# Kernel optimization log

Hardware: AMD Instinct MI355X
Metric: run time of the kernel (lower is better)

Reference implementation:

```python
import jax, jax.numpy as jnp
import numpy as np

# Dimensions
B, NIN, P, K, D, F = 8, 4096, 1024, 16, 2, 64
CPF, C, DM = 64, 128, 2
CIN = CPF + F
BN_EPS = 1e-3  # Keras BatchNormalization default epsilon


def _bn(x, prm):
    # inference-mode batchnorm; prm is (4, C): gamma, beta, moving_mean, moving_var
    g, b, m, v = prm
    return g * (x - m) * jax.lax.rsqrt(v + BN_EPS) + b


def setup_inputs() -> dict:
    key = jax.random.key(0)
    ks = jax.random.split(key, 24)
    s = 0.05
    def rn(k, shape):
        return jax.random.normal(k, shape, jnp.float32) * s
    def bn_prm(k, c):
        kg, kb, km, kv = jax.random.split(k, 4)
        return jnp.stack([
            1.0 + 0.1 * jax.random.normal(kg, (c,), jnp.float32),
            0.1 * jax.random.normal(kb, (c,), jnp.float32),
            0.1 * jax.random.normal(km, (c,), jnp.float32),
            jax.random.uniform(kv, (c,), jnp.float32, 0.5, 1.5),
        ])
    inputs = jax.random.normal(ks[0], (B, NIN, 3 + F), jnp.float32)
    return {
        "inputs": inputs,
        "W_pf1": rn(ks[1], (3, CPF)), "b_pf1": rn(ks[2], (CPF,)), "bn_pf1": bn_prm(ks[3], CPF),
        "W_pf2": rn(ks[4], (CPF, CPF)), "b_pf2": rn(ks[5], (CPF,)), "bn_pf2": bn_prm(ks[6], CPF),
        "W_c1": rn(ks[7], (K, 3, K * K)), "b_c1": rn(ks[8], (K * K,)), "bn_c1": bn_prm(ks[9], K * K),
        "W_c2": rn(ks[10], (K, K, K)), "b_c2": rn(ks[11], (K * K,)), "bn_c2": bn_prm(ks[12], K * K),
        "W_c3": rn(ks[13], (K, K, K)), "b_c3": rn(ks[14], (K * K,)), "bn_c3": bn_prm(ks[15], K * K),
        "W_df": rn(ks[16], (K, CIN, DM)), "W_pw": rn(ks[17], (CIN * DM, C)),
        "b_f": rn(ks[18], (C,)), "bn_f": bn_prm(ks[19], C),
    }


def reference(inputs, W_pf1, b_pf1, bn_pf1, W_pf2, b_pf2, bn_pf2,
              W_c1, b_c1, bn_c1, W_c2, b_c2, bn_c2, W_c3, b_c3, bn_c3,
              W_df, W_pw, b_f, bn_f):
    p = inputs[:, :, :3]              # (B, NIN, 3) positions
    q = p[:, :P, :]                   # (B, P, 3) 'random' sampled query points
    # knn_indices_general(q, p, K*D, sorted=True): squared-distance top-k
    d2 = (q * q).sum(-1)[:, :, None] + (p * p).sum(-1)[:, None, :] \
         - 2.0 * jnp.einsum('bqc,bpc->bqp', q, p)          # (B, P, NIN)
    _, idx_kd = jax.lax.top_k(-d2, K * D)                  # ascending distance
    idx = idx_kd[:, :, ::D]                                # dilation -> (B, P, K)
    gathered = jnp.take_along_axis(
        inputs, idx.reshape(B, P * K)[:, :, None], axis=1).reshape(B, P, K, 3 + F)
    p_nb = gathered[..., :3] - q[:, :, None, :]            # (B, P, K, 3) local coords
    f_nb = gathered[..., 3:]                               # (B, P, K, F)
    # pos -> feature: Dense, BN, Dense, BN (no activation in source)
    h = _bn(p_nb @ W_pf1 + b_pf1, bn_pf1)
    h = _bn(h @ W_pf2 + b_pf2, bn_pf2)
    feat = jnp.concatenate([h, f_nb], axis=-1)             # (B, P, K, CIN)
    # Conv2D(K*K, (1,K), elu) + BN: contraction over neighbor axis
    x = _bn(jax.nn.elu(jnp.einsum('bnjc,jco->bno', p_nb, W_c1) + b_c1), bn_c1)
    x = x.reshape(B, P, K, K)
    # DepthwiseConv2D((1,K), mult=K, elu) + BN; Keras channel order c*mult+m
    x = _bn(jax.nn.elu(jnp.einsum('bnwc,wcm->bncm', x, W_c2).reshape(B, P, K * K) + b_c2), bn_c2)
    x = x.reshape(B, P, K, K)
    x = _bn(jax.nn.elu(jnp.einsum('bnwc,wcm->bncm', x, W_c3).reshape(B, P, K * K) + b_c3), bn_c3)
    x = x.reshape(B, P, K, K)
    # per-point KxK X-transform on gathered features
    feat = jnp.einsum('bnij,bnjc->bnic', x, feat)          # (B, P, K, CIN)
    # SeparableConv2D(C, (1,K), mult=DM, elu) + BN; width axis collapses
    dw = jnp.einsum('bnjc,jcm->bncm', feat, W_df).reshape(B, P, CIN * DM)
    out = _bn(jax.nn.elu(dw @ W_pw + b_f), bn_f)           # (B, P, C)
    return jnp.concatenate([q, out], axis=-1)              # (B, P, 3 + C)
```

## Files before the change

kernel.cpp:

```cpp
#include <hip/hip_runtime.h>
#include <math.h>

#define B_    8
#define NIN_  4096
#define P_    1024
#define K_    16
#define F_    64
#define CH_   67
#define CPF_  64
#define CIN_  128
#define C_    128

#define S_PF1  0
#define SH_PF1 64
#define S_PF2  128
#define SH_PF2 192
#define S_C1   256
#define SH_C1  512
#define S_C2   768
#define SH_C2  1024
#define S_C3   1280
#define SH_C3  1536
#define S_F    1792
#define SH_F   1920
#define M_OFF  2048
#define C0_OFF 2240

#define WS_PTS_OFF  16384
#define WS_IDX_OFF  (WS_PTS_OFF + B_ * NIN_ * 16)
#define WS_DWL_OFF  (WS_IDX_OFF + B_ * P_ * K_ * 4)

__device__ __forceinline__ float rlf(float x, int l) {
    return __int_as_float(__builtin_amdgcn_readlane(__float_as_int(x), l));
}
__device__ __forceinline__ float eluf(float z) {
    return z > 0.f ? z : expm1f(z);
}
__device__ __forceinline__ float dpp_shr1_f(float x) {
    return __int_as_float(__builtin_amdgcn_update_dpp(
        __float_as_int(x), __float_as_int(x), 0x138, 0xF, 0xF, false));
}
__device__ __forceinline__ int dpp_shr1_i(int x) {
    return __builtin_amdgcn_update_dpp(x, x, 0x138, 0xF, 0xF, false);
}

__global__ void bn_prep(const float* __restrict__ bn_pf1, const float* __restrict__ bn_pf2,
                        const float* __restrict__ bn_c1,  const float* __restrict__ bn_c2,
                        const float* __restrict__ bn_c3,  const float* __restrict__ bn_f,
                        const float* __restrict__ Wpf1,   const float* __restrict__ bpf1,
                        const float* __restrict__ Wpf2,   const float* __restrict__ bpf2,
                        float* __restrict__ wsf) {
    int t = threadIdx.x;
    {
        const float* src; int nch, c, so, sho;
        if (t < 64)       { src = bn_pf1; nch = 64;  c = t;        so = S_PF1; sho = SH_PF1; }
        else if (t < 128) { src = bn_pf2; nch = 64;  c = t - 64;   so = S_PF2; sho = SH_PF2; }
        else if (t < 384) { src = bn_c1;  nch = 256; c = t - 128;  so = S_C1;  sho = SH_C1; }
        else if (t < 640) { src = bn_c2;  nch = 256; c = t - 384;  so = S_C2;  sho = SH_C2; }
        else if (t < 896) { src = bn_c3;  nch = 256; c = t - 640;  so = S_C3;  sho = SH_C3; }
        else              { src = bn_f;   nch = 128; c = t - 896;  so = S_F;   sho = SH_F;  }
        float g = src[c], b = src[nch + c], m = src[2 * nch + c], v = src[3 * nch + c];
        float s = g * rsqrtf(v + 1e-3f);
        wsf[so + c]  = s;
        wsf[sho + c] = b - m * s;
    }
    __syncthreads();
    if (t < 64) {
        int o = t;
        float s2 = wsf[S_PF2 + o], t2 = wsf[SH_PF2 + o];
        float m0 = 0.f, m1 = 0.f, m2 = 0.f, cc = 0.f;
        for (int c = 0; c < 64; ++c) {
            float s1 = wsf[S_PF1 + c], t1 = wsf[SH_PF1 + c];
            float d1 = s1 * bpf1[c] + t1;
            float w2 = Wpf2[c * 64 + o];
            m0 += Wpf1[0 * 64 + c] * s1 * w2;
            m1 += Wpf1[1 * 64 + c] * s1 * w2;
            m2 += Wpf1[2 * 64 + c] * s1 * w2;
            cc += d1 * w2;
        }
        wsf[M_OFF + 0 * 64 + o] = m0 * s2;
        wsf[M_OFF + 1 * 64 + o] = m1 * s2;
        wsf[M_OFF + 2 * 64 + o] = m2 * s2;
        wsf[C0_OFF + o]         = cc * s2 + bpf2[o] * s2 + t2;
    }
}

__global__ __launch_bounds__(256) void pack_pts(const float* __restrict__ inp,
                                                float4* __restrict__ pts) {
    int i = blockIdx.x * 256 + threadIdx.x;
    if (i < B_ * NIN_) {
        const float* r = inp + (size_t)i * CH_;
        float x = r[0], y = r[1], z = r[2];
        float pp = __fadd_rn(__fadd_rn(__fmul_rn(x, x), __fmul_rn(y, y)),
                             __fmul_rn(z, z));
        pts[i] = make_float4(x, y, z, pp);
    }
}

__global__ __launch_bounds__(256) void knn_kernel(const float4* __restrict__ pts,
                                                  int* __restrict__ idxo) {
    const int wid  = (blockIdx.x << 2) | (threadIdx.x >> 6);
    const int lane = threadIdx.x & 63;
    const float4* bp = pts + ((size_t)(wid >> 10) << 12);
    const int qi = wid & 1023;

    const float4 q = bp[qi];
    const float qq = q.w;

    float4 p = bp[lane];
    float d;
    {
        float e = __fadd_rn(__fadd_rn(__fmul_rn(q.x, p.x), __fmul_rn(q.y, p.y)),
                            __fmul_rn(q.z, p.z));
        d = __fsub_rn(__fadd_rn(qq, p.w), __fmul_rn(2.0f, e));
    }
    int ii = lane;
#pragma unroll
    for (int k = 2; k <= 64; k <<= 1) {
#pragma unroll
        for (int j = k >> 1; j > 0; j >>= 1) {
            float od = __shfl_xor(d, j);
            int   oi = __shfl_xor(ii, j);
            bool keepmin = (((lane & k) == 0) == ((lane & j) == 0));
            bool ol = (od < d) || (od == d && oi < ii);
            bool take = keepmin ? ol : !ol;
            if (take) { d = od; ii = oi; }
        }
    }
    float bd = d;
    int   bi = ii;
    float kth = rlf(bd, 31);

    float4 pn = bp[64 + lane];
    for (int j0 = 64; j0 < NIN_; j0 += 64) {
        p = pn;
        if (j0 + 64 < NIN_) pn = bp[j0 + 64 + lane];
        float e  = __fadd_rn(__fadd_rn(__fmul_rn(q.x, p.x), __fmul_rn(q.y, p.y)),
                             __fmul_rn(q.z, p.z));
        float d2 = __fsub_rn(__fadd_rn(qq, p.w), __fmul_rn(2.0f, e));

        unsigned long long m = __ballot(d2 < kth);
        if (m) {
            do {
                int c = __builtin_ctzll(m);
                m &= m - 1;
                float dc = rlf(d2, c);
                int   ic = j0 + c;
                float prev  = dpp_shr1_f(bd);
                int   previ = dpp_shr1_i(bi);
                bool  shift = (bd > dc);
                bool  ins   = shift && ((lane == 0) || (prev <= dc));
                if (shift) { bd = prev; bi = previ; }
                if (ins)   { bd = dc;   bi = ic;    }
            } while (m);
            kth = rlf(bd, 31);
        }
    }

    if (lane < 32 && !(lane & 1)) {
        idxo[((size_t)wid << 4) | (lane >> 1)] = bi;
    }
}

__global__ __launch_bounds__(256) void p1_kernel(
    const float* __restrict__ inp, const int* __restrict__ idx,
    const float* __restrict__ Wc1,  const float* __restrict__ bc1,
    const float* __restrict__ Wc2,  const float* __restrict__ bc2,
    const float* __restrict__ Wc3,  const float* __restrict__ bc3,
    const float* __restrict__ Wdf,  const float* __restrict__ wsf,
    float* __restrict__ dwl, float* __restrict__ out) {

    __shared__ float xS[4][2][256];
    __shared__ float yS[4][2][256];

    const int w   = threadIdx.x >> 6;
    const int l   = threadIdx.x & 63;
    const int ngA = blockIdx.x * 8 + w * 2;
    const int ngB = ngA + 1;
    const int b   = ngA >> 10;
    const float* brow = inp + (size_t)b * NIN_ * CH_;
    const int* ipA = idx + (size_t)ngA * K_;
    const int* ipB = idx + (size_t)ngB * K_;

    const int nA = ngA & 1023, nB = ngB & 1023;
    const float q0A = brow[(size_t)nA * CH_ + 0];
    const float q1A = brow[(size_t)nA * CH_ + 1];
    const float q2A = brow[(size_t)nA * CH_ + 2];
    const float q0B = brow[(size_t)nB * CH_ + 0];
    const float q1B = brow[(size_t)nB * CH_ + 1];
    const float q2B = brow[(size_t)nB * CH_ + 2];

    float pdA, pdB;
    {
        int k3 = (l * 21846) >> 16;
        k3 = (k3 > 15) ? 15 : k3;
        int d3 = l - ((k3 << 1) + k3);
        d3 = (d3 > 2) ? 2 : d3;
        int nblA = ipA[k3];
        int nblB = ipB[k3];
        float vA = 0.f, vB = 0.f;
        if (l < 48) {
            vA = brow[(size_t)nblA * CH_ + d3];
            vB = brow[(size_t)nblB * CH_ + d3];
        }
        float qvA = (d3 == 0) ? q0A : ((d3 == 1) ? q1A : q2A);
        float qvB = (d3 == 0) ? q0B : ((d3 == 1) ? q1B : q2B);
        pdA = vA - qvA;
        pdB = vB - qvB;
    }

    {
        float4 accA = *reinterpret_cast<const float4*>(bc1 + 4 * l);
        float4 accB = accA;
#pragma unroll 4
        for (int t4 = 0; t4 < 12; ++t4) {
            const float* wb = Wc1 + (size_t)(t4 * 4) * 256 + 4 * l;
            float4 w0 = *reinterpret_cast<const float4*>(wb);
            float4 w1 = *reinterpret_cast<const float4*>(wb + 256);
            float4 w2 = *reinterpret_cast<const float4*>(wb + 512);
            float4 w3 = *reinterpret_cast<const float4*>(wb + 768);
            float a0 = rlf(pdA, 4 * t4 + 0), a1 = rlf(pdA, 4 * t4 + 1);
            float a2 = rlf(pdA, 4 * t4 + 2), a3 = rlf(pdA, 4 * t4 + 3);
            accA.x += a0 * w0.x + a1 * w1.x + a2 * w2.x + a3 * w3.x;
            accA.y += a0 * w0.y + a1 * w1.y + a2 * w2.y + a3 * w3.y;
            accA.z += a0 * w0.z + a1 * w1.z + a2 * w2.z + a3 * w3.z;
            accA.w += a0 * w0.w + a1 * w1.w + a2 * w2.w + a3 * w3.w;
            float e0 = rlf(pdB, 4 * t4 + 0), e1 = rlf(pdB, 4 * t4 + 1);
            float e2 = rlf(pdB, 4 * t4 + 2), e3 = rlf(pdB, 4 * t4 + 3);
            accB.x += e0 * w0.x + e1 * w1.x + e2 * w2.x + e3 * w3.x;
            accB.y += e0 * w0.y + e1 * w1.y + e2 * w2.y + e3 * w3.y;
            accB.z += e0 * w0.z + e1 * w1.z + e2 * w2.z + e3 * w3.z;
            accB.w += e0 * w0.w + e1 * w1.w + e2 * w2.w + e3 * w3.w;
        }
        float4 sc = *reinterpret_cast<const float4*>(wsf + S_C1 + 4 * l);
        float4 sh = *reinterpret_cast<const float4*>(wsf + SH_C1 + 4 * l);
        float4 rA, rB;
        rA.x = sc.x * eluf(accA.x) + sh.x;  rB.x = sc.x * eluf(accB.x) + sh.x;
        rA.y = sc.y * eluf(accA.y) + sh.y;  rB.y = sc.y * eluf(accB.y) + sh.y;
        rA.z = sc.z * eluf(accA.z) + sh.z;  rB.z = sc.z * eluf(accB.z) + sh.z;
        rA.w = sc.w * eluf(accA.w) + sh.w;  rB.w = sc.w * eluf(accB.w) + sh.w;
        *reinterpret_cast<float4*>(&xS[w][0][4 * l]) = rA;
        *reinterpret_cast<float4*>(&xS[w][1][4 * l]) = rB;
    }

    {
        float4 accA = *reinterpret_cast<const float4*>(bc2 + 4 * l);
        float4 accB = accA;
        const int csel = l >> 2;
#pragma unroll 8
        for (int w16 = 0; w16 < 16; ++w16) {
            float4 w4 = *reinterpret_cast<const float4*>(Wc2 + (size_t)w16 * 256 + 4 * l);
            float xa = xS[w][0][w16 * 16 + csel];
            float xb = xS[w][1][w16 * 16 + csel];
            accA.x += xa * w4.x; accA.y += xa * w4.y;
            accA.z += xa * w4.z; accA.w += xa * w4.w;
            accB.x += xb * w4.x; accB.y += xb * w4.y;
            accB.z += xb * w4.z; accB.w += xb * w4.w;
        }
        float4 sc = *reinterpret_cast<const float4*>(wsf + S_C2 + 4 * l);
        float4 sh = *reinterpret_cast<const float4*>(wsf + SH_C2 + 4 * l);
        float4 rA, rB;
        rA.x = sc.x * eluf(accA.x) + sh.x;  rB.x = sc.x * eluf(accB.x) + sh.x;
        rA.y = sc.y * eluf(accA.y) + sh.y;  rB.y = sc.y * eluf(accB.y) + sh.y;
        rA.z = sc.z * eluf(accA.z) + sh.z;  rB.z = sc.z * eluf(accB.z) + sh.z;
        rA.w = sc.w * eluf(accA.w) + sh.w;  rB.w = sc.w * eluf(accB.w) + sh.w;
        *reinterpret_cast<float4*>(&yS[w][0][4 * l]) = rA;
        *reinterpret_cast<float4*>(&yS[w][1][4 * l]) = rB;
    }

    float x3A[4], x3B[4];
    {
        float4 accA = *reinterpret_cast<const float4*>(bc3 + 4 * l);
        float4 accB = accA;
        const int csel = l >> 2;
#pragma unroll 8
        for (int w16 = 0; w16 < 16; ++w16) {
            float4 w4 = *reinterpret_cast<const float4*>(Wc3 + (size_t)w16 * 256 + 4 * l);
            float xa = yS[w][0][w16 * 16 + csel];
            float xb = yS[w][1][w16 * 16 + csel];
            accA.x += xa * w4.x; accA.y += xa * w4.y;
            accA.z += xa * w4.z; accA.w += xa * w4.w;
            accB.x += xb * w4.x; accB.y += xb * w4.y;
            accB.z += xb * w4.z; accB.w += xb * w4.w;
        }
        float4 sc = *reinterpret_cast<const float4*>(wsf + S_C3 + 4 * l);
        float4 sh = *reinterpret_cast<const float4*>(wsf + SH_C3 + 4 * l);
        x3A[0] = sc.x * eluf(accA.x) + sh.x;  x3B[0] = sc.x * eluf(accB.x) + sh.x;
        x3A[1] = sc.y * eluf(accA.y) + sh.y;  x3B[1] = sc.y * eluf(accB.y) + sh.y;
        x3A[2] = sc.z * eluf(accA.z) + sh.z;  x3B[2] = sc.z * eluf(accB.z) + sh.z;
        x3A[3] = sc.w * eluf(accA.w) + sh.w;  x3B[3] = sc.w * eluf(accB.w) + sh.w;
    }

    const float Mw0 = wsf[M_OFF + l];
    const float Mw1 = wsf[M_OFF + 64 + l];
    const float Mw2 = wsf[M_OFF + 128 + l];
    const float cc0 = wsf[C0_OFF + l];

    float fnbA[16];
#pragma unroll
    for (int k = 0; k < 16; ++k) {
        int nbs = __builtin_amdgcn_readfirstlane(ipA[k]);
        fnbA[k] = brow[(size_t)nbs * CH_ + 3 + l];
    }
    float h2A[16];
#pragma unroll
    for (int k = 0; k < 16; ++k) {
        float s0 = rlf(pdA, 3 * k), s1 = rlf(pdA, 3 * k + 1), s2 = rlf(pdA, 3 * k + 2);
        h2A[k] = fmaf(s0, Mw0, fmaf(s1, Mw1, fmaf(s2, Mw2, cc0)));
    }
    float fnbB[16];
#pragma unroll
    for (int k = 0; k < 16; ++k) {
        int nbs = __builtin_amdgcn_readfirstlane(ipB[k]);
        fnbB[k] = brow[(size_t)nbs * CH_ + 3 + l];
    }
    {
        float d00 = 0.f, d01 = 0.f, d10 = 0.f, d11 = 0.f;
#pragma unroll 4
        for (int i = 0; i < 16; ++i) {
            float fa = 0.f, fb = 0.f;
#pragma unroll
            for (int j = 0; j < 16; ++j) {
                float xv = rlf(x3A[j & 3], i * 4 + (j >> 2));
                fa += xv * h2A[j];
                fb += xv * fnbA[j];
            }
            const float* wr = Wdf + (size_t)i * 256;
            float2 wlo = *reinterpret_cast<const float2*>(wr + 2 * l);
            float2 whi = *reinterpret_cast<const float2*>(wr + 128 + 2 * l);
            d00 += fa * wlo.x; d01 += fa * wlo.y;
            d10 += fb * whi.x; d11 += fb * whi.y;
        }
        float* drow = dwl + (size_t)ngA * 256;
        *reinterpret_cast<float2*>(drow + 2 * l)       = make_float2(d00, d01);
        *reinterpret_cast<float2*>(drow + 128 + 2 * l) = make_float2(d10, d11);
    }

    float h2B[16];
#pragma unroll
    for (int k = 0; k < 16; ++k) {
        float s0 = rlf(pdB, 3 * k), s1 = rlf(pdB, 3 * k + 1), s2 = rlf(pdB, 3 * k + 2);
        h2B[k] = fmaf(s0, Mw0, fmaf(s1, Mw1, fmaf(s2, Mw2, cc0)));
    }
    {
        float d00 = 0.f, d01 = 0.f, d10 = 0.f, d11 = 0.f;
#pragma unroll 4
        for (int i = 0; i < 16; ++i) {
            float fa = 0.f, fb = 0.f;
#pragma unroll
            for (int j = 0; j < 16; ++j) {
                float xv = rlf(x3B[j & 3], i * 4 + (j >> 2));
                fa += xv * h2B[j];
                fb += xv * fnbB[j];
            }
            const float* wr = Wdf + (size_t)i * 256;
            float2 wlo = *reinterpret_cast<const float2*>(wr + 2 * l);
            float2 whi = *reinterpret_cast<const float2*>(wr + 128 + 2 * l);
            d00 += fa * wlo.x; d01 += fa * wlo.y;
            d10 += fb * whi.x; d11 += fb * whi.y;
        }
        float* drow = dwl + (size_t)ngB * 256;
        *reinterpret_cast<float2*>(drow + 2 * l)       = make_float2(d00, d01);
        *reinterpret_cast<float2*>(drow + 128 + 2 * l) = make_float2(d10, d11);
    }

    if (l < 3) {
        out[(size_t)ngA * 131 + l] = (l == 0) ? q0A : ((l == 1) ? q1A : q2A);
        out[(size_t)ngB * 131 + l] = (l == 0) ? q0B : ((l == 1) ? q1B : q2B);
    }
}

__global__ __launch_bounds__(256) void pw_kernel(const float* __restrict__ dwl,
                                                 const float* __restrict__ Wpw,
                                                 const float* __restrict__ bf,
                                                 const float* __restrict__ wsf,
                                                 float* __restrict__ out) {
    __shared__ float As[32][256];
    const int tid = threadIdx.x;
    const int m0  = blockIdx.x * 32;

#pragma unroll
    for (int i = 0; i < 8; ++i) {
        int fi  = i * 1024 + tid * 4;
        int row = fi >> 8, col = fi & 255;
        *reinterpret_cast<float4*>(&As[row][col]) =
            *reinterpret_cast<const float4*>(dwl + (size_t)(m0 + row) * 256 + col);
    }
    __syncthreads();

    const int mq = tid >> 5;
    const int nq = tid & 31;
    float acc[4][4];
#pragma unroll
    for (int mi = 0; mi < 4; ++mi)
#pragma unroll
        for (int ni = 0; ni < 4; ++ni) acc[mi][ni] = 0.f;

#pragma unroll 4
    for (int k4 = 0; k4 < 64; ++k4) {
        float4 a[4], bw[4];
#pragma unroll
        for (int mi = 0; mi < 4; ++mi)
            a[mi] = *reinterpret_cast<const float4*>(&As[mq * 4 + mi][k4 * 4]);
#pragma unroll
        for (int ki = 0; ki < 4; ++ki)
            bw[ki] = *reinterpret_cast<const float4*>(Wpw + (size_t)(k4 * 4 + ki) * 128 + nq * 4);
#pragma unroll
        for (int mi = 0; mi < 4; ++mi) {
            const float4 am = a[mi];
            acc[mi][0] += am.x * bw[0].x + am.y * bw[1].x + am.z * bw[2].x + am.w * bw[3].x;
            acc[mi][1] += am.x * bw[0].y + am.y * bw[1].y + am.z * bw[2].y + am.w * bw[3].y;
            acc[mi][2] += am.x * bw[0].z + am.y * bw[1].z + am.z * bw[2].z + am.w * bw[3].z;
            acc[mi][3] += am.x * bw[0].w + am.y * bw[1].w + am.z * bw[2].w + am.w * bw[3].w;
        }
    }

    float4 b4  = *reinterpret_cast<const float4*>(bf + nq * 4);
    float4 sc4 = *reinterpret_cast<const float4*>(wsf + S_F + nq * 4);
    float4 sh4 = *reinterpret_cast<const float4*>(wsf + SH_F + nq * 4);
#pragma unroll
    for (int mi = 0; mi < 4; ++mi) {
        const int m = m0 + mq * 4 + mi;
        float* orow = out + (size_t)m * 131 + 3 + nq * 4;
        orow[0] = sc4.x * eluf(acc[mi][0] + b4.x) + sh4.x;
        orow[1] = sc4.y * eluf(acc[mi][1] + b4.y) + sh4.y;
        orow[2] = sc4.z * eluf(acc[mi][2] + b4.z) + sh4.z;
        orow[3] = sc4.w * eluf(acc[mi][3] + b4.w) + sh4.w;
    }
}

extern "C" void kernel_launch(void* const* d_in, const int* in_sizes, int n_in,
                              void* d_out, int out_size, void* d_ws, size_t ws_size,
                              hipStream_t stream) {
    const float* inp   = (const float*)d_in[0];
    const float* Wpf1  = (const float*)d_in[1];
    const float* bpf1  = (const float*)d_in[2];
    const float* bnpf1 = (const float*)d_in[3];
    const float* Wpf2  = (const float*)d_in[4];
    const float* bpf2  = (const float*)d_in[5];
    const float* bnpf2 = (const float*)d_in[6];
    const float* Wc1   = (const float*)d_in[7];
    const float* bc1   = (const float*)d_in[8];
    const float* bnc1  = (const float*)d_in[9];
    const float* Wc2   = (const float*)d_in[10];
    const float* bc2   = (const float*)d_in[11];
    const float* bnc2  = (const float*)d_in[12];
    const float* Wc3   = (const float*)d_in[13];
    const float* bc3   = (const float*)d_in[14];
    const float* bnc3  = (const float*)d_in[15];
    const float* Wdf   = (const float*)d_in[16];
    const float* Wpw   = (const float*)d_in[17];
    const float* bf    = (const float*)d_in[18];
    const float* bnf   = (const float*)d_in[19];

    float*  wsf  = (float*)d_ws;
    float4* pts  = (float4*)((char*)d_ws + WS_PTS_OFF);
    int*    idxw = (int*)((char*)d_ws + WS_IDX_OFF);
    float*  dwl  = (float*)((char*)d_ws + WS_DWL_OFF);
    float*  outp = (float*)d_out;

    hipLaunchKernelGGL(bn_prep, dim3(1), dim3(1024), 0, stream,
                       bnpf1, bnpf2, bnc1, bnc2, bnc3, bnf,
                       Wpf1, bpf1, Wpf2, bpf2, wsf);
    hipLaunchKernelGGL(pack_pts, dim3((B_ * NIN_ + 255) / 256), dim3(256), 0, stream,
                       inp, pts);
    hipLaunchKernelGGL(knn_kernel, dim3((B_ * P_) / 4), dim3(256), 0, stream,
                       pts, idxw);
    hipLaunchKernelGGL(p1_kernel, dim3((B_ * P_) / 8), dim3(256), 0, stream,
                       inp, idxw, Wc1, bc1, Wc2, bc2, Wc3, bc3, Wdf, wsf,
                       dwl, outp);
    hipLaunchKernelGGL(pw_kernel, dim3((B_ * P_) / 32), dim3(256), 0, stream,
                       dwl, Wpw, bf, wsf, outp);
}
```

Measured before the change: 125.9 us.

## Merge prep kernels, deepen kNN prefetch, make insertion step branchless

Combines the BN-parameter preparation and point packing into one launch: the first 128 blocks pack points and one extra block folds the BN parameters. The kNN scan now prefetches two 64-point chunks per iteration. The sorted-list insertion uses a DPP shift filled with -inf together with fmin/fmax selects instead of divergent branches. Together these aim to cut launch overhead, global-load latency and per-insertion instruction count, at the cost of more registers in the kNN kernel.

```diff
diff --git a/kernel.cpp b/kernel.cpp
--- a/kernel.cpp
+++ b/kernel.cpp
@@ -36,22 +36,35 @@
 __device__ __forceinline__ float eluf(float z) {
     return z > 0.f ? z : expm1f(z);
 }
-__device__ __forceinline__ float dpp_shr1_f(float x) {
+__device__ __forceinline__ float dpp_shr1_ninf(float x) {
     return __int_as_float(__builtin_amdgcn_update_dpp(
-        __float_as_int(x), __float_as_int(x), 0x138, 0xF, 0xF, false));
+        (int)0xFF800000, __float_as_int(x), 0x138, 0xF, 0xF, false));
 }
 __device__ __forceinline__ int dpp_shr1_i(int x) {
     return __builtin_amdgcn_update_dpp(x, x, 0x138, 0xF, 0xF, false);
 }
 
-__global__ void bn_prep(const float* __restrict__ bn_pf1, const float* __restrict__ bn_pf2,
-                        const float* __restrict__ bn_c1,  const float* __restrict__ bn_c2,
-                        const float* __restrict__ bn_c3,  const float* __restrict__ bn_f,
-                        const float* __restrict__ Wpf1,   const float* __restrict__ bpf1,
-                        const float* __restrict__ Wpf2,   const float* __restrict__ bpf2,
-                        float* __restrict__ wsf) {
-    int t = threadIdx.x;
-    {
+__global__ __launch_bounds__(256) void prep_kernel(
+    const float* __restrict__ inp, float4* __restrict__ pts,
+    const float* __restrict__ bn_pf1, const float* __restrict__ bn_pf2,
+    const float* __restrict__ bn_c1,  const float* __restrict__ bn_c2,
+    const float* __restrict__ bn_c3,  const float* __restrict__ bn_f,
+    const float* __restrict__ Wpf1,   const float* __restrict__ bpf1,
+    const float* __restrict__ Wpf2,   const float* __restrict__ bpf2,
+    float* __restrict__ wsf) {
+    const int tid = threadIdx.x;
+    if (blockIdx.x < 128) {
+        int i = blockIdx.x * 256 + tid;
+        const float* r = inp + (size_t)i * CH_;
+        float x = r[0], y = r[1], z = r[2];
+        float pp = __fadd_rn(__fadd_rn(__fmul_rn(x, x), __fmul_rn(y, y)),
+                             __fmul_rn(z, z));
+        pts[i] = make_float4(x, y, z, pp);
+        return;
+    }
+#pragma unroll
+    for (int it = 0; it < 4; ++it) {
+        int t = it * 256 + tid;
         const float* src; int nch, c, so, sho;
         if (t < 64)       { src = bn_pf1; nch = 64;  c = t;        so = S_PF1; sho = SH_PF1; }
         else if (t < 128) { src = bn_pf2; nch = 64;  c = t - 64;   so = S_PF2; sho = SH_PF2; }
@@ -65,8 +78,8 @@
         wsf[sho + c] = b - m * s;
     }
     __syncthreads();
-    if (t < 64) {
-        int o = t;
+    if (tid < 64) {
+        int o = tid;
         float s2 = wsf[S_PF2 + o], t2 = wsf[SH_PF2 + o];
         float m0 = 0.f, m1 = 0.f, m2 = 0.f, cc = 0.f;
         for (int c = 0; c < 64; ++c) {
@@ -85,18 +98,6 @@
     }
 }
 
-__global__ __launch_bounds__(256) void pack_pts(const float* __restrict__ inp,
-                                                float4* __restrict__ pts) {
-    int i = blockIdx.x * 256 + threadIdx.x;
-    if (i < B_ * NIN_) {
-        const float* r = inp + (size_t)i * CH_;
-        float x = r[0], y = r[1], z = r[2];
-        float pp = __fadd_rn(__fadd_rn(__fmul_rn(x, x), __fmul_rn(y, y)),
-                             __fmul_rn(z, z));
-        pts[i] = make_float4(x, y, z, pp);
-    }
-}
-
 __global__ __launch_bounds__(256) void knn_kernel(const float4* __restrict__ pts,
                                                   int* __restrict__ idxo) {
     const int wid  = (blockIdx.x << 2) | (threadIdx.x >> 6);
@@ -107,13 +108,16 @@
     const float4 q = bp[qi];
     const float qq = q.w;
 
-    float4 p = bp[lane];
-    float d;
-    {
-        float e = __fadd_rn(__fadd_rn(__fmul_rn(q.x, p.x), __fmul_rn(q.y, p.y)),
-                            __fmul_rn(q.z, p.z));
-        d = __fsub_rn(__fadd_rn(qq, p.w), __fmul_rn(2.0f, e));
-    }
+#define DIST2(P) __fsub_rn(__fadd_rn(qq, (P).w), __fmul_rn(2.0f, \
+    __fadd_rn(__fadd_rn(__fmul_rn(q.x, (P).x), __fmul_rn(q.y, (P).y)), \
+              __fmul_rn(q.z, (P).z))))
+
+    float4 p  = bp[lane];
+    float4 g1 = bp[64 + lane];
+    float4 g2 = bp[128 + lane];
+    float4 g3 = bp[192 + lane];
+
+    float d = DIST2(p);
     int ii = lane;
 #pragma unroll
     for (int k = 2; k <= 64; k <<= 1) {
@@ -131,31 +135,41 @@
     int   bi = ii;
     float kth = rlf(bd, 31);
 
-    float4 pn = bp[64 + lane];
-    for (int j0 = 64; j0 < NIN_; j0 += 64) {
-        p = pn;
-        if (j0 + 64 < NIN_) pn = bp[j0 + 64 + lane];
-        float e  = __fadd_rn(__fadd_rn(__fmul_rn(q.x, p.x), __fmul_rn(q.y, p.y)),
-                             __fmul_rn(q.z, p.z));
-        float d2 = __fsub_rn(__fadd_rn(qq, p.w), __fmul_rn(2.0f, e));
-
+#define INS_LOOP(MV, D2V, BASE)                                        \
+    if (MV) {                                                          \
+        do {                                                           \
+            int c = (int)__builtin_ctzll(MV); MV &= MV - 1;            \
+            float dc = rlf(D2V, c);                                    \
+            int   ic = (BASE) + c;                                     \
+            float prev  = dpp_shr1_ninf(bd);                           \
+            int   previ = dpp_shr1_i(bi);                              \
+            bool c1 = (bd > dc);                                       \
+            bool c2 = (prev > dc);                                     \
+            bd = fminf(bd, fmaxf(prev, dc));                           \
+            bi = c1 ? (c2 ? previ : ic) : bi;                          \
+        } while (MV);                                                  \
+        kth = rlf(bd, 31);                                             \
+    }
+
+    {
+        float d2 = DIST2(g1);
         unsigned long long m = __ballot(d2 < kth);
-        if (m) {
-            do {
-                int c = __builtin_ctzll(m);
-                m &= m - 1;
-                float dc = rlf(d2, c);
-                int   ic = j0 + c;
-                float prev  = dpp_shr1_f(bd);
-                int   previ = dpp_shr1_i(bi);
-                bool  shift = (bd > dc);
-                bool  ins   = shift && ((lane == 0) || (prev <= dc));
-                if (shift) { bd = prev; bi = previ; }
-                if (ins)   { bd = dc;   bi = ic;    }
-            } while (m);
-            kth = rlf(bd, 31);
-        }
-    }
+        INS_LOOP(m, d2, 64);
+    }
+
+    for (int j0 = 128; j0 < NIN_; j0 += 128) {
+        float4 pa = g2, pb = g3;
+        int jn = j0 + 128;
+        if (jn < NIN_) { g2 = bp[jn + lane]; g3 = bp[jn + 64 + lane]; }
+        float d2a = DIST2(pa);
+        unsigned long long ma = __ballot(d2a < kth);
+        INS_LOOP(ma, d2a, j0);
+        float d2b = DIST2(pb);
+        unsigned long long mb = __ballot(d2b < kth);
+        INS_LOOP(mb, d2b, j0 + 64);
+    }
+#undef INS_LOOP
+#undef DIST2
 
     if (lane < 32 && !(lane & 1)) {
         idxo[((size_t)wid << 4) | (lane >> 1)] = bi;
@@ -459,11 +473,9 @@
     float*  dwl  = (float*)((char*)d_ws + WS_DWL_OFF);
     float*  outp = (float*)d_out;
 
-    hipLaunchKernelGGL(bn_prep, dim3(1), dim3(1024), 0, stream,
-                       bnpf1, bnpf2, bnc1, bnc2, bnc3, bnf,
+    hipLaunchKernelGGL(prep_kernel, dim3(129), dim3(256), 0, stream,
+                       inp, pts, bnpf1, bnpf2, bnc1, bnc2, bnc3, bnf,
                        Wpf1, bpf1, Wpf2, bpf2, wsf);
-    hipLaunchKernelGGL(pack_pts, dim3((B_ * NIN_ + 255) / 256), dim3(256), 0, stream,
-                       inp, pts);
     hipLaunchKernelGGL(knn_kernel, dim3((B_ * P_) / 4), dim3(256), 0, stream,
                        pts, idxw);
     hipLaunchKernelGGL(p1_kernel, dim3((B_ * P_) / 8), dim3(256), 0, stream,
```

Result: no change. 125.5 us (-0.3%).
